# Optimization experiments

Measured on AMD Instinct MI355X. Metric: run time of the kernel, lower is better.

The kernel has to match this reference:

```python
import jax, jax.numpy as jnp
import numpy as np

EMB = 64
L = 2
NU = 100000
NI = 50000
ER = 1000000
ET = 800000
EP = 200000


def setup_inputs() -> dict:
    key = jax.random.key(0)
    ks = jax.random.split(key, 32)
    f = jnp.float32
    def nrm(k, shape, s=0.01):
        return (jax.random.normal(k, shape) * s).astype(f)
    inp = {}
    # graph structure (int)
    inp['rate_src'] = jax.random.randint(ks[0], (ER,), 0, NU)
    inp['rate_dst'] = jax.random.randint(ks[1], (ER,), 0, NI)
    inp['trust_src'] = jax.random.randint(ks[2], (ET,), 0, NU)
    inp['trust_dst'] = jax.random.randint(ks[3], (ET,), 0, NU)
    inp['pos_u'] = jax.random.randint(ks[4], (EP,), 0, NU)
    inp['pos_i'] = jax.random.randint(ks[5], (EP,), 0, NI)
    inp['neg_u'] = jax.random.randint(ks[6], (EP,), 0, NU)
    inp['neg_i'] = jax.random.randint(ks[7], (EP,), 0, NI)
    # embeddings (init normal(0, 0.01) per init_weights)
    inp['eu'] = nrm(ks[8], (NU, EMB))
    inp['ei'] = nrm(ks[9], (NI, EMB))
    # per-rel GATv2 params, stacked over L layers; [:,0]=fc_src, [:,1]=fc_dst
    inp['rate_W'] = nrm(ks[10], (L, 2, EMB, EMB))
    inp['rate_b'] = jnp.zeros((L, 2, EMB), f)
    inp['rate_attn'] = nrm(ks[11], (L, EMB), 0.1)
    inp['rate_bias'] = jnp.zeros((L, EMB), f)
    inp['rb_W'] = nrm(ks[12], (L, 2, EMB, EMB))
    inp['rb_b'] = jnp.zeros((L, 2, EMB), f)
    inp['rb_attn'] = nrm(ks[13], (L, EMB), 0.1)
    inp['rb_bias'] = jnp.zeros((L, EMB), f)
    inp['tr_W'] = nrm(ks[14], (L, 2, EMB, EMB))
    inp['tr_b'] = jnp.zeros((L, 2, EMB), f)
    inp['tr_attn'] = nrm(ks[15], (L, EMB), 0.1)
    inp['tr_bias'] = jnp.zeros((L, EMB), f)
    # attention-gate MLPs: [:, 0]=influence, [:, 1]=interest
    inp['attW1'] = nrm(ks[16], (L, 2, 2 * EMB, 2 * EMB))
    inp['attb1'] = jnp.zeros((L, 2, 2 * EMB), f)
    inp['attW2'] = nrm(ks[17], (L, 2, 2 * EMB))
    inp['attb2'] = jnp.zeros((L, 2), f)
    return inp


def gatv2(hs, hd, src, dst, Ws, bs, Wd, bd, attn, bias, n_dst):
    # DGL GATv2Conv, num_heads=1: e = attn . leaky_relu(Ws h_u + Wd h_v), slope 0.2
    fs = hs @ Ws + bs          # [Ns, E]
    fd = hd @ Wd + bd          # [Nd, E]
    e = jax.nn.leaky_relu(fs[src] + fd[dst], 0.2) @ attn  # [E]
    m = jax.ops.segment_max(e, dst, num_segments=n_dst)
    ex = jnp.exp(e - m[dst])
    denom = jax.ops.segment_sum(ex, dst, num_segments=n_dst)
    alpha = ex / denom[dst]
    out = jax.ops.segment_sum(alpha[:, None] * fs[src], dst, num_segments=n_dst)
    return out + bias


def _bn1(x):
    # BatchNorm1d(1), training-mode batch stats, affine identity at init
    mu = jnp.mean(x)
    var = jnp.mean((x - mu) ** 2)
    return (x - mu) * jax.lax.rsqrt(var + 1e-5)


def reference(eu, ei, rate_W, rate_b, rate_attn, rate_bias, rb_W, rb_b, rb_attn,
              rb_bias, tr_W, tr_b, tr_attn, tr_bias, attW1, attb1, attW2, attb2,
              rate_src, rate_dst, trust_src, trust_dst, pos_u, pos_i, neg_u, neg_i):
    n_users, n_items = eu.shape[0], ei.shape[0]
    hu, hi = eu, ei
    res_u, res_i = [eu], [ei]
    for l in range(rate_W.shape[0]):
        # interest diffusion: rate (user->item) and rated-by (item->user, reverse edges)
        hi_new = gatv2(hu, hi, rate_src, rate_dst, rate_W[l, 0], rate_b[l, 0],
                       rate_W[l, 1], rate_b[l, 1], rate_attn[l], rate_bias[l], n_items) + hi
        q = gatv2(hi, hu, rate_dst, rate_src, rb_W[l, 0], rb_b[l, 0],
                  rb_W[l, 1], rb_b[l, 1], rb_attn[l], rb_bias[l], n_users)
        # influence diffusion: trust (user->user)
        p = gatv2(hu, hu, trust_src, trust_dst, tr_W[l, 0], tr_b[l, 0],
                  tr_W[l, 1], tr_b[l, 1], tr_attn[l], tr_bias[l], n_users)
        def att(h2, i):
            z = (h2 @ attW1[l, i] + attb1[l, i]) @ attW2[l, i] + attb2[l, i]  # [N]
            return jax.nn.leaky_relu(_bn1(z), 0.01)
        a_inf = att(jnp.concatenate([hu, p], axis=1), 0)
        a_int = att(jnp.concatenate([hu, q], axis=1), 1)
        gamma = jax.nn.softmax(jnp.stack([a_inf, a_int], axis=1), axis=1)  # [N,2]
        hu = gamma[:, 0:1] * p + gamma[:, 1:2] * q + hu
        hi = hi_new
        res_u.append(hu)
        res_i.append(hi)
    hu_all = jnp.concatenate(res_u, axis=1)  # [NU, EMB*(1+L)]
    hi_all = jnp.concatenate(res_i, axis=1)
    pos = jnp.sum(hu_all[pos_u] * hi_all[pos_i], axis=1, keepdims=True)  # [EP,1]
    neg = jnp.sum(hu_all[neg_u] * hi_all[neg_i], axis=1, keepdims=True)
    return pos, neg
```

## Files before the change

kernel.cpp:

```cpp
#include <hip/hip_runtime.h>
#include <hip/hip_bf16.h>
#include <cstdint>

typedef __hip_bfloat16 bf16;
typedef __attribute__((ext_vector_type(8))) short frag_ab;
typedef __attribute__((ext_vector_type(4))) float frag_cd;
typedef __attribute__((ext_vector_type(4))) short short4v;

__device__ __forceinline__ float b2f(short s){
  return __uint_as_float(((unsigned)(unsigned short)s) << 16);
}

__device__ __forceinline__ void bf_split(float x, short& hi, short& lo){
  bf16 h = __float2bfloat16(x);
  float hf = __bfloat162float(h);
  bf16 l = __float2bfloat16(x - hf);
  __builtin_memcpy(&hi, &h, 2);
  __builtin_memcpy(&lo, &l, 2);
}

__device__ __forceinline__ float wave_sum(float v){
#pragma unroll
  for (int o = 32; o > 0; o >>= 1) v += __shfl_down(v, o, 64);
  return v;
}

__global__ void k_copy_in(const float* __restrict__ src, float* __restrict__ dst,
                          int n, int stride){
  int idx = blockIdx.x * 256 + threadIdx.x;
  if (idx >= n * 64) return;
  int r = idx >> 6, j = idx & 63;
  dst[(size_t)r * stride + j] = src[idx];
}

__global__ void k_linear(const float* __restrict__ x, int xs, int xo,
                         const float* __restrict__ W, const float* __restrict__ b,
                         bf16* __restrict__ out, int n){
  __shared__ float Wl[4096];
  int t = threadIdx.x;
  for (int i = t; i < 4096; i += 256) Wl[i] = W[i];
  __syncthreads();
  int lane = t & 63, w = t >> 6;
  int quad = lane >> 4, n16 = lane & 15;

  frag_ab bhi[4][2], blo[4][2];
#pragma unroll
  for (int c = 0; c < 4; ++c)
#pragma unroll
    for (int h = 0; h < 2; ++h){
      frag_ab vh, vl;
#pragma unroll
      for (int j = 0; j < 8; ++j){
        float wv = Wl[(32 * h + quad * 8 + j) * 64 + 16 * c + n16];
        short sh, sl; bf_split(wv, sh, sl);
        vh[j] = sh; vl[j] = sl;
      }
      bhi[c][h] = vh; blo[c][h] = vl;
    }
  float bj[4];
#pragma unroll
  for (int c = 0; c < 4; ++c) bj[c] = b[16 * c + n16];

  int rowbase = blockIdx.x * 64 + w * 16;
  if (rowbase >= n) return;
  int lrow = rowbase + n16; if (lrow >= n) lrow = n - 1;
  const float* xp = x + (size_t)lrow * xs + xo;
  frag_ab ahi[2], alo[2];
#pragma unroll
  for (int h = 0; h < 2; ++h){
    frag_ab vh, vl;
#pragma unroll
    for (int j = 0; j < 8; ++j){
      float xv = xp[32 * h + quad * 8 + j];
      short sh, sl; bf_split(xv, sh, sl);
      vh[j] = sh; vl[j] = sl;
    }
    ahi[h] = vh; alo[h] = vl;
  }
  frag_cd acc[4];
#pragma unroll
  for (int c = 0; c < 4; ++c) acc[c] = frag_cd{0.f, 0.f, 0.f, 0.f};
#pragma unroll
  for (int c = 0; c < 4; ++c)
#pragma unroll
    for (int h = 0; h < 2; ++h){
      acc[c] = __builtin_amdgcn_mfma_f32_16x16x32_bf16(ahi[h], bhi[c][h], acc[c], 0, 0, 0);
      acc[c] = __builtin_amdgcn_mfma_f32_16x16x32_bf16(alo[h], bhi[c][h], acc[c], 0, 0, 0);
      acc[c] = __builtin_amdgcn_mfma_f32_16x16x32_bf16(ahi[h], blo[c][h], acc[c], 0, 0, 0);
    }
#pragma unroll
  for (int reg = 0; reg < 4; ++reg){
    int r = rowbase + quad * 4 + reg;
    if (r >= n) continue;
#pragma unroll
    for (int c = 0; c < 4; ++c)
      out[(size_t)r * 64 + 16 * c + n16] = __float2bfloat16(acc[c][reg] + bj[c]);
  }
}

__global__ void k_hist(const int* __restrict__ dst, int* __restrict__ cnt, int E){
  int k = blockIdx.x * 256 + threadIdx.x;
  if (k < E) atomicAdd(cnt + dst[k], 1);
}
__global__ void k_hist2(const int* __restrict__ src, const int* __restrict__ dst,
                        int* __restrict__ cntA, int* __restrict__ cntB, int E){
  int k = blockIdx.x * 256 + threadIdx.x;
  if (k >= E) return;
  atomicAdd(cntA + dst[k], 1);
  atomicAdd(cntB + src[k], 1);
}

__global__ void k_scan_mb(const int* __restrict__ cnt, int n,
                          int* __restrict__ offs, int* __restrict__ cur,
                          int* __restrict__ gbase){
  __shared__ int wsum[16];
  __shared__ int base_sh;
  int t = threadIdx.x, lane = t & 63, w = t >> 6;
  int i = blockIdx.x * 1024 + t;
  int v = (i < n) ? cnt[i] : 0;
  int x = v;
#pragma unroll
  for (int o = 1; o < 64; o <<= 1){
    int y = __shfl_up(x, o, 64);
    if (lane >= o) x += y;
  }
  if (lane == 63) wsum[w] = x;
  __syncthreads();
  if (t == 0){
    int tot = 0;
    for (int k = 0; k < 16; ++k){ int c = wsum[k]; wsum[k] = tot; tot += c; }
    base_sh = atomicAdd(gbase, tot);
  }
  __syncthreads();
  if (i < n){
    int e = base_sh + wsum[w] + x - v;
    offs[i] = e; cur[i] = e;
  }
}

__global__ void k_csr_fill(const int* __restrict__ src, const int* __restrict__ dst,
                           int* __restrict__ cur, int* __restrict__ csr_src, int E){
  int t = blockIdx.x * 256 + threadIdx.x;
  int T = gridDim.x * 256;
  int k0 = t, k1 = t + T, k2 = t + 2 * T, k3 = t + 3 * T;
  bool b0 = k0 < E, b1 = k1 < E, b2 = k2 < E, b3 = k3 < E;
  int s0 = 0, d0 = 0, s1 = 0, d1 = 0, s2 = 0, d2 = 0, s3 = 0, d3 = 0;
  if (b0){ s0 = src[k0]; d0 = dst[k0]; }
  if (b1){ s1 = src[k1]; d1 = dst[k1]; }
  if (b2){ s2 = src[k2]; d2 = dst[k2]; }
  if (b3){ s3 = src[k3]; d3 = dst[k3]; }
  int p0 = 0, p1 = 0, p2 = 0, p3 = 0;
  if (b0) p0 = atomicAdd(cur + d0, 1);
  if (b1) p1 = atomicAdd(cur + d1, 1);
  if (b2) p2 = atomicAdd(cur + d2, 1);
  if (b3) p3 = atomicAdd(cur + d3, 1);
  if (b0) csr_src[p0] = s0;
  if (b1) csr_src[p1] = s1;
  if (b2) csr_src[p2] = s2;
  if (b3) csr_src[p3] = s3;
}
__global__ void k_csr_fill2(const int* __restrict__ src, const int* __restrict__ dst,
                            int* __restrict__ curA, int* __restrict__ csrA,
                            int* __restrict__ curB, int* __restrict__ csrB, int E){
  int t = blockIdx.x * 256 + threadIdx.x;
  int T = gridDim.x * 256;
  int k0 = t, k1 = t + T, k2 = t + 2 * T, k3 = t + 3 * T;
  bool b0 = k0 < E, b1 = k1 < E, b2 = k2 < E, b3 = k3 < E;
  int s0 = 0, d0 = 0, s1 = 0, d1 = 0, s2 = 0, d2 = 0, s3 = 0, d3 = 0;
  if (b0){ s0 = src[k0]; d0 = dst[k0]; }
  if (b1){ s1 = src[k1]; d1 = dst[k1]; }
  if (b2){ s2 = src[k2]; d2 = dst[k2]; }
  if (b3){ s3 = src[k3]; d3 = dst[k3]; }
  int pa0 = 0, pa1 = 0, pa2 = 0, pa3 = 0, pb0 = 0, pb1 = 0, pb2 = 0, pb3 = 0;
  if (b0) pa0 = atomicAdd(curA + d0, 1);
  if (b1) pa1 = atomicAdd(curA + d1, 1);
  if (b2) pa2 = atomicAdd(curA + d2, 1);
  if (b3) pa3 = atomicAdd(curA + d3, 1);
  if (b0) pb0 = atomicAdd(curB + s0, 1);
  if (b1) pb1 = atomicAdd(curB + s1, 1);
  if (b2) pb2 = atomicAdd(curB + s2, 1);
  if (b3) pb3 = atomicAdd(curB + s3, 1);
  if (b0){ csrA[pa0] = s0; csrB[pb0] = d0; }
  if (b1){ csrA[pa1] = s1; csrB[pb1] = d1; }
  if (b2){ csrA[pa2] = s2; csrB[pb2] = d2; }
  if (b3){ csrA[pa3] = s3; csrB[pb3] = d3; }
}

__global__ void k_gat(const int* __restrict__ offs, const int* __restrict__ cnt,
                      const int* __restrict__ csr_src,
                      const bf16* __restrict__ fs, const bf16* __restrict__ fd,
                      const float* __restrict__ attn, const float* __restrict__ bias,
                      float* __restrict__ out, int os, int oo,
                      const float* __restrict__ res, int rs, int ro, int n){
  int d = blockIdx.x * 4 + (threadIdx.x >> 6);
  if (d >= n) return;
  int lane = threadIdx.x & 63;
  int g = lane >> 4, l16 = lane & 15;
  short4v dv = *(const short4v*)(fd + (size_t)d * 64 + 4 * l16);
  float fd0 = b2f(dv[0]), fd1 = b2f(dv[1]), fd2 = b2f(dv[2]), fd3 = b2f(dv[3]);
  float4 a4 = *(const float4*)(attn + 4 * l16);
  float acc0 = 0.f, acc1 = 0.f, acc2 = 0.f, acc3 = 0.f, den = 0.f;
  int idx0 = offs[d], end = idx0 + cnt[d];
  for (int idx = idx0; idx < end; idx += 4){
    int e = idx + g;
    bool valid = e < end;
    int s = csr_src[valid ? e : idx];
    short4v sv = *(const short4v*)(fs + (size_t)s * 64 + 4 * l16);
    float f0 = b2f(sv[0]), f1 = b2f(sv[1]), f2 = b2f(sv[2]), f3 = b2f(sv[3]);
    float v0 = f0 + fd0; v0 = (v0 > 0.f ? v0 : 0.2f * v0) * a4.x;
    float v1 = f1 + fd1; v1 = (v1 > 0.f ? v1 : 0.2f * v1) * a4.y;
    float v2 = f2 + fd2; v2 = (v2 > 0.f ? v2 : 0.2f * v2) * a4.z;
    float v3 = f3 + fd3; v3 = (v3 > 0.f ? v3 : 0.2f * v3) * a4.w;
    float tt = (v0 + v1) + (v2 + v3);
#pragma unroll
    for (int o = 1; o < 16; o <<= 1) tt += __shfl_xor(tt, o, 64);
    float ex = valid ? __expf(tt) : 0.f;
    acc0 += ex * f0; acc1 += ex * f1; acc2 += ex * f2; acc3 += ex * f3;
    den += ex;
  }
#pragma unroll
  for (int o = 16; o < 64; o <<= 1){
    acc0 += __shfl_xor(acc0, o, 64); acc1 += __shfl_xor(acc1, o, 64);
    acc2 += __shfl_xor(acc2, o, 64); acc3 += __shfl_xor(acc3, o, 64);
    den  += __shfl_xor(den, o, 64);
  }
  if (g == 0){
    float4 b4 = *(const float4*)(bias + 4 * l16);
    float inv = (den > 0.f) ? 1.f / den : 0.f;
    float o0 = acc0 * inv + b4.x, o1 = acc1 * inv + b4.y;
    float o2 = acc2 * inv + b4.z, o3 = acc3 * inv + b4.w;
    if (res){
      float4 r4 = *(const float4*)(res + (size_t)d * rs + ro + 4 * l16);
      o0 += r4.x; o1 += r4.y; o2 += r4.z; o3 += r4.w;
    }
    *(float4*)(out + (size_t)d * os + oo + 4 * l16) = make_float4(o0, o1, o2, o3);
  }
}

__global__ void k_attvec(const float* __restrict__ W1, const float* __restrict__ b1,
                         const float* __restrict__ W2, const float* __restrict__ b2,
                         float* __restrict__ vvec, float* __restrict__ cs){
  int t = threadIdx.x;
  int li = t >> 7, r = t & 127;
  float acc = 0.f;
  for (int c = 0; c < 128; ++c)
    acc += W1[(size_t)(li * 128 + r) * 128 + c] * W2[li * 128 + c];
  vvec[li * 128 + r] = acc;
  if (r == 0){
    float cacc = b2[li];
    for (int c = 0; c < 128; ++c)
      cacc += b1[li * 128 + c] * W2[li * 128 + c];
    cs[li] = cacc;
  }
}

__global__ void k_gate_z(const float* __restrict__ hu_all, int l,
                         const float* __restrict__ p, const float* __restrict__ q,
                         const float* __restrict__ vvec, const float* __restrict__ cs,
                         float* __restrict__ z1, float* __restrict__ z2,
                         float* __restrict__ bsums, int n){
  __shared__ float part[4][4];
  int w = threadIdx.x >> 6, j = threadIdx.x & 63;
  int nidx = blockIdx.x * 4 + w;
  float lz1 = 0.f, lz2 = 0.f;
  if (nidx < n){
    const float* v1 = vvec + l * 256;
    const float* v2 = vvec + l * 256 + 128;
    float h  = hu_all[(size_t)nidx * 192 + l * 64 + j];
    float pv = p[(size_t)nidx * 64 + j];
    float qv = q[(size_t)nidx * 64 + j];
    float t1 = wave_sum(h * v1[j] + pv * v1[64 + j]);
    float t2 = wave_sum(h * v2[j] + qv * v2[64 + j]);
    if (j == 0){
      lz1 = t1 + cs[l * 2 + 0];
      lz2 = t2 + cs[l * 2 + 1];
      z1[nidx] = lz1;
      z2[nidx] = lz2;
    }
  }
  if (j == 0){
    part[w][0] = lz1; part[w][1] = lz1 * lz1;
    part[w][2] = lz2; part[w][3] = lz2 * lz2;
  }
  __syncthreads();
  if (threadIdx.x < 4)
    bsums[(size_t)blockIdx.x * 4 + threadIdx.x] =
        part[0][threadIdx.x] + part[1][threadIdx.x] +
        part[2][threadIdx.x] + part[3][threadIdx.x];
}

__global__ void k_bn_part(const float* __restrict__ bsums, int nb,
                          double* __restrict__ gpart){
  __shared__ double sh[256];
  int c = threadIdx.x & 3, r0 = blockIdx.x * 64 + (threadIdx.x >> 2);
  double acc = 0.0;
  for (int i = r0; i < nb; i += gridDim.x * 64)
    acc += (double)bsums[(size_t)i * 4 + c];
  sh[threadIdx.x] = acc;
  __syncthreads();
  for (int s = 128; s >= 4; s >>= 1){
    if (threadIdx.x < s) sh[threadIdx.x] += sh[threadIdx.x + s];
    __syncthreads();
  }
  if (threadIdx.x < 4) gpart[(size_t)blockIdx.x * 4 + threadIdx.x] = sh[threadIdx.x];
}

__global__ void k_bn_final(const double* __restrict__ gpart, int nbk,
                           double* __restrict__ sums){
  __shared__ double sh[256];
  int c = threadIdx.x & 3, k0 = threadIdx.x >> 2;
  double acc = 0.0;
  for (int i = k0; i < nbk; i += 64) acc += gpart[(size_t)i * 4 + c];
  sh[threadIdx.x] = acc;
  __syncthreads();
  for (int s = 128; s >= 4; s >>= 1){
    if (threadIdx.x < s) sh[threadIdx.x] += sh[threadIdx.x + s];
    __syncthreads();
  }
  if (threadIdx.x < 4) sums[threadIdx.x] = sh[threadIdx.x];
}

__global__ void k_gate_combine(float* __restrict__ hu_all, int l,
                               const float* __restrict__ p, const float* __restrict__ q,
                               const float* __restrict__ z1, const float* __restrict__ z2,
                               const double* __restrict__ sums, int n){
  int idx = blockIdx.x * 256 + threadIdx.x;
  if (idx >= n * 64) return;
  int r = idx >> 6, j = idx & 63;
  double invn = 1.0 / (double)n;
  double mu1 = sums[0] * invn, mu2 = sums[2] * invn;
  float var1 = (float)(sums[1] * invn - mu1 * mu1);
  float var2 = (float)(sums[3] * invn - mu2 * mu2);
  float rs1 = rsqrtf(var1 + 1e-5f), rs2 = rsqrtf(var2 + 1e-5f);
  float a1 = (z1[r] - (float)mu1) * rs1;
  float a2 = (z2[r] - (float)mu2) * rs2;
  a1 = a1 > 0.f ? a1 : 0.01f * a1;
  a2 = a2 > 0.f ? a2 : 0.01f * a2;
  float mx = fmaxf(a1, a2);
  float e1 = __expf(a1 - mx), e2 = __expf(a2 - mx);
  float inv = 1.f / (e1 + e2);
  float out = (e1 * inv) * p[idx] + (e2 * inv) * q[idx]
            + hu_all[(size_t)r * 192 + l * 64 + j];
  hu_all[(size_t)r * 192 + (l + 1) * 64 + j] = out;
}

__global__ void k_score(const int* __restrict__ pu, const int* __restrict__ pi,
                        const int* __restrict__ nu, const int* __restrict__ ni,
                        const float* __restrict__ hu_all, const float* __restrict__ hi_all,
                        float* __restrict__ out, int EP){
  int gw = blockIdx.x * 4 + (threadIdx.x >> 6);
  int sub = (threadIdx.x >> 4) & 3, l16 = threadIdx.x & 15;
  int k = gw * 4 + sub;
  if (k >= 2 * EP) return;
  int u, i;
  if (k < EP){ u = pu[k]; i = pi[k]; } else { u = nu[k - EP]; i = ni[k - EP]; }
  const float4* hu = (const float4*)(hu_all + (size_t)u * 192);
  const float4* hi = (const float4*)(hi_all + (size_t)i * 192);
  float acc = 0.f;
#pragma unroll
  for (int t = 0; t < 3; ++t){
    float4 a = hu[l16 + 16 * t];
    float4 b = hi[l16 + 16 * t];
    acc += a.x * b.x + a.y * b.y + a.z * b.z + a.w * b.w;
  }
#pragma unroll
  for (int o = 8; o > 0; o >>= 1) acc += __shfl_xor(acc, o, 64);
  if (l16 == 0) out[k] = acc;
}

extern "C" void kernel_launch(void* const* d_in, const int* in_sizes, int n_in,
                              void* d_out, int out_size, void* d_ws, size_t ws_size,
                              hipStream_t stream) {
  const int*   rate_src  = (const int*)  d_in[0];
  const int*   rate_dst  = (const int*)  d_in[1];
  const int*   trust_src = (const int*)  d_in[2];
  const int*   trust_dst = (const int*)  d_in[3];
  const int*   pos_u     = (const int*)  d_in[4];
  const int*   pos_i     = (const int*)  d_in[5];
  const int*   neg_u     = (const int*)  d_in[6];
  const int*   neg_i     = (const int*)  d_in[7];
  const float* eu        = (const float*)d_in[8];
  const float* ei        = (const float*)d_in[9];
  const float* rate_W    = (const float*)d_in[10];
  const float* rate_b    = (const float*)d_in[11];
  const float* rate_attn = (const float*)d_in[12];
  const float* rate_bias = (const float*)d_in[13];
  const float* rb_W      = (const float*)d_in[14];
  const float* rb_b      = (const float*)d_in[15];
  const float* rb_attn   = (const float*)d_in[16];
  const float* rb_bias   = (const float*)d_in[17];
  const float* tr_W      = (const float*)d_in[18];
  const float* tr_b      = (const float*)d_in[19];
  const float* tr_attn   = (const float*)d_in[20];
  const float* tr_bias   = (const float*)d_in[21];
  const float* attW1     = (const float*)d_in[22];
  const float* attb1     = (const float*)d_in[23];
  const float* attW2     = (const float*)d_in[24];
  const float* attb2     = (const float*)d_in[25];

  const int ER = in_sizes[0];
  const int ET = in_sizes[2];
  const int EP = in_sizes[4];
  const int NU = in_sizes[8] / 64;
  const int NI = in_sizes[9] / 64;

  float* ws = (float*)d_ws;
  float*  hu_all = ws;
  float*  hi_all = hu_all + (size_t)NU * 192;
  float*  p      = hi_all + (size_t)NI * 192;
  float*  q      = p + (size_t)NU * 64;
  bf16*   fs     = (bf16*)(q + (size_t)NU * 64);
  bf16*   fd     = (bf16*)(q + (size_t)NU * 128);
  float*  z1     = q + (size_t)NU * 192;
  float*  z2     = z1 + NU;
  float*  bsums  = z2 + NU;
  float*  vvec   = bsums + (size_t)(((NU + 3) / 4) * 4);
  float*  cs     = vvec + 512;
  double* sums   = (double*)(((uintptr_t)(cs + 4) + 15) & ~(uintptr_t)15);
  double* gpart  = sums + 4;
  int*    iw     = (int*)(gpart + 512);
  int*    cntA   = iw;
  int*    cntB   = cntA + NI;
  int*    cntC   = cntB + NU;
  int*    gbase  = cntC + NU;
  int*    offsA  = gbase + 4;
  int*    curA   = offsA + NI;
  int*    offsB  = curA + NI;
  int*    curB   = offsB + NU;
  int*    offsC  = curB + NU;
  int*    curC   = offsC + NU;
  int*    csrA   = curC + NU;
  int*    csrB   = csrA + ER;
  int*    csrC   = csrB + ER;

  auto cdiv = [](int a, int b){ return (a + b - 1) / b; };
  const int nbz = cdiv(NU, 4);

  k_copy_in<<<cdiv(NU * 64, 256), 256, 0, stream>>>(eu, hu_all, NU, 192);
  k_copy_in<<<cdiv(NI * 64, 256), 256, 0, stream>>>(ei, hi_all, NI, 192);
  k_attvec<<<1, 512, 0, stream>>>(attW1, attb1, attW2, attb2, vvec, cs);

  hipMemsetAsync(cntA, 0, (size_t)(NI + 2 * NU + 4) * 4, stream);
  k_hist2<<<cdiv(ER, 256), 256, 0, stream>>>(rate_src, rate_dst, cntA, cntB, ER);
  k_hist<<<cdiv(ET, 256), 256, 0, stream>>>(trust_dst, cntC, ET);
  k_scan_mb<<<cdiv(NI, 1024), 1024, 0, stream>>>(cntA, NI, offsA, curA, gbase + 0);
  k_scan_mb<<<cdiv(NU, 1024), 1024, 0, stream>>>(cntB, NU, offsB, curB, gbase + 1);
  k_scan_mb<<<cdiv(NU, 1024), 1024, 0, stream>>>(cntC, NU, offsC, curC, gbase + 2);
  k_csr_fill2<<<cdiv(ER, 1024), 256, 0, stream>>>(rate_src, rate_dst,
      curA, csrA, curB, csrB, ER);
  k_csr_fill<<<cdiv(ET, 1024), 256, 0, stream>>>(trust_src, trust_dst, curC, csrC, ET);

  for (int l = 0; l < 2; ++l){
    k_linear<<<cdiv(NU, 64), 256, 0, stream>>>(hu_all, 192, l * 64,
        rate_W + (size_t)(l * 2 + 0) * 4096, rate_b + (l * 2 + 0) * 64, fs, NU);
    k_linear<<<cdiv(NI, 64), 256, 0, stream>>>(hi_all, 192, l * 64,
        rate_W + (size_t)(l * 2 + 1) * 4096, rate_b + (l * 2 + 1) * 64, fd, NI);
    k_gat<<<cdiv(NI, 4), 256, 0, stream>>>(offsA, cntA, csrA, fs, fd,
        rate_attn + l * 64, rate_bias + l * 64,
        hi_all, 192, (l + 1) * 64, hi_all, 192, l * 64, NI);

    k_linear<<<cdiv(NI, 64), 256, 0, stream>>>(hi_all, 192, l * 64,
        rb_W + (size_t)(l * 2 + 0) * 4096, rb_b + (l * 2 + 0) * 64, fs, NI);
    k_linear<<<cdiv(NU, 64), 256, 0, stream>>>(hu_all, 192, l * 64,
        rb_W + (size_t)(l * 2 + 1) * 4096, rb_b + (l * 2 + 1) * 64, fd, NU);
    k_gat<<<cdiv(NU, 4), 256, 0, stream>>>(offsB, cntB, csrB, fs, fd,
        rb_attn + l * 64, rb_bias + l * 64,
        q, 64, 0, (const float*)nullptr, 0, 0, NU);

    k_linear<<<cdiv(NU, 64), 256, 0, stream>>>(hu_all, 192, l * 64,
        tr_W + (size_t)(l * 2 + 0) * 4096, tr_b + (l * 2 + 0) * 64, fs, NU);
    k_linear<<<cdiv(NU, 64), 256, 0, stream>>>(hu_all, 192, l * 64,
        tr_W + (size_t)(l * 2 + 1) * 4096, tr_b + (l * 2 + 1) * 64, fd, NU);
    k_gat<<<cdiv(NU, 4), 256, 0, stream>>>(offsC, cntC, csrC, fs, fd,
        tr_attn + l * 64, tr_bias + l * 64,
        p, 64, 0, (const float*)nullptr, 0, 0, NU);

    k_gate_z<<<nbz, 256, 0, stream>>>(hu_all, l, p, q, vvec, cs, z1, z2, bsums, NU);
    k_bn_part<<<128, 256, 0, stream>>>(bsums, nbz, gpart);
    k_bn_final<<<1, 256, 0, stream>>>(gpart, 128, sums);
    k_gate_combine<<<cdiv(NU * 64, 256), 256, 0, stream>>>(hu_all, l, p, q, z1, z2, sums, NU);
  }

  k_score<<<cdiv(2 * EP, 16), 256, 0, stream>>>(pos_u, pos_i, neg_u, neg_i,
      hu_all, hi_all, (float*)d_out, EP);
}
```

Measured before the change: 1.070 ms.

## Batch linear projections per input, pre-split weights, and drop second CSR atomic pass

```diff
diff --git a/kernel.cpp b/kernel.cpp
--- a/kernel.cpp
+++ b/kernel.cpp
@@ -10,7 +10,6 @@
 __device__ __forceinline__ float b2f(short s){
   return __uint_as_float(((unsigned)(unsigned short)s) << 16);
 }
-
 __device__ __forceinline__ void bf_split(float x, short& hi, short& lo){
   bf16 h = __float2bfloat16(x);
   float hf = __bfloat162float(h);
@@ -33,34 +32,31 @@
   dst[(size_t)r * stride + j] = src[idx];
 }
 
-__global__ void k_linear(const float* __restrict__ x, int xs, int xo,
-                         const float* __restrict__ W, const float* __restrict__ b,
-                         bf16* __restrict__ out, int n){
-  __shared__ float Wl[4096];
-  int t = threadIdx.x;
-  for (int i = t; i < 4096; i += 256) Wl[i] = W[i];
-  __syncthreads();
-  int lane = t & 63, w = t >> 6;
+__global__ void k_wsplit(const float* __restrict__ rateW, const float* __restrict__ rbW,
+                         const float* __restrict__ trW,
+                         short* __restrict__ Whi, short* __restrict__ Wlo){
+  int tid = blockIdx.x * 256 + threadIdx.x;
+  if (tid >= 12 * 4096) return;
+  int m = tid >> 12, rem = tid & 4095;
+  int lane = rem >> 6, rem2 = rem & 63;
+  int pair = rem2 >> 3, j = rem2 & 7;
+  int c = pair >> 1, h = pair & 1;
+  int rel = m >> 2, li = m & 3;
+  const float* base = (rel == 0) ? rateW : (rel == 1) ? rbW : trW;
+  float v = base[(size_t)li * 4096 + (32 * h + (lane >> 4) * 8 + j) * 64 + 16 * c + (lane & 15)];
+  short sh, sl; bf_split(v, sh, sl);
+  Whi[tid] = sh; Wlo[tid] = sl;
+}
+
+__global__ void k_linear_multi(const float* __restrict__ x, int xs, int xo, int n,
+                               const short* __restrict__ Whi, const short* __restrict__ Wlo,
+                               int mcount,
+                               int m0, const float* __restrict__ b0, bf16* __restrict__ o0,
+                               int m1, const float* __restrict__ b1, bf16* __restrict__ o1,
+                               int m2, const float* __restrict__ b2, bf16* __restrict__ o2,
+                               int m3, const float* __restrict__ b3, bf16* __restrict__ o3){
+  int lane = threadIdx.x & 63, w = threadIdx.x >> 6;
   int quad = lane >> 4, n16 = lane & 15;
-
-  frag_ab bhi[4][2], blo[4][2];
-#pragma unroll
-  for (int c = 0; c < 4; ++c)
-#pragma unroll
-    for (int h = 0; h < 2; ++h){
-      frag_ab vh, vl;
-#pragma unroll
-      for (int j = 0; j < 8; ++j){
-        float wv = Wl[(32 * h + quad * 8 + j) * 64 + 16 * c + n16];
-        short sh, sl; bf_split(wv, sh, sl);
-        vh[j] = sh; vl[j] = sl;
-      }
-      bhi[c][h] = vh; blo[c][h] = vl;
-    }
-  float bj[4];
-#pragma unroll
-  for (int c = 0; c < 4; ++c) bj[c] = b[16 * c + n16];
-
   int rowbase = blockIdx.x * 64 + w * 16;
   if (rowbase >= n) return;
   int lrow = rowbase + n16; if (lrow >= n) lrow = n - 1;
@@ -77,42 +73,54 @@
     }
     ahi[h] = vh; alo[h] = vl;
   }
-  frag_cd acc[4];
-#pragma unroll
-  for (int c = 0; c < 4; ++c) acc[c] = frag_cd{0.f, 0.f, 0.f, 0.f};
-#pragma unroll
-  for (int c = 0; c < 4; ++c)
-#pragma unroll
-    for (int h = 0; h < 2; ++h){
-      acc[c] = __builtin_amdgcn_mfma_f32_16x16x32_bf16(ahi[h], bhi[c][h], acc[c], 0, 0, 0);
-      acc[c] = __builtin_amdgcn_mfma_f32_16x16x32_bf16(alo[h], bhi[c][h], acc[c], 0, 0, 0);
-      acc[c] = __builtin_amdgcn_mfma_f32_16x16x32_bf16(ahi[h], blo[c][h], acc[c], 0, 0, 0);
+  int ms[4] = {m0, m1, m2, m3};
+  const float* bs[4] = {b0, b1, b2, b3};
+  bf16* os[4] = {o0, o1, o2, o3};
+  for (int i = 0; i < mcount; ++i){
+    const frag_ab* Bh = (const frag_ab*)(Whi + (size_t)ms[i] * 4096 + lane * 64);
+    const frag_ab* Bl = (const frag_ab*)(Wlo + (size_t)ms[i] * 4096 + lane * 64);
+    frag_cd acc[4];
+#pragma unroll
+    for (int c = 0; c < 4; ++c) acc[c] = frag_cd{0.f, 0.f, 0.f, 0.f};
+#pragma unroll
+    for (int c = 0; c < 4; ++c)
+#pragma unroll
+      for (int h = 0; h < 2; ++h){
+        frag_ab bh = Bh[c * 2 + h], bl = Bl[c * 2 + h];
+        acc[c] = __builtin_amdgcn_mfma_f32_16x16x32_bf16(ahi[h], bh, acc[c], 0, 0, 0);
+        acc[c] = __builtin_amdgcn_mfma_f32_16x16x32_bf16(alo[h], bh, acc[c], 0, 0, 0);
+        acc[c] = __builtin_amdgcn_mfma_f32_16x16x32_bf16(ahi[h], bl, acc[c], 0, 0, 0);
+      }
+    const float* bb = bs[i];
+    bf16* oo = os[i];
+#pragma unroll
+    for (int reg = 0; reg < 4; ++reg){
+      int r = rowbase + quad * 4 + reg;
+      if (r >= n) continue;
+#pragma unroll
+      for (int c = 0; c < 4; ++c)
+        oo[(size_t)r * 64 + 16 * c + n16] = __float2bfloat16(acc[c][reg] + bb[16 * c + n16]);
     }
-#pragma unroll
-  for (int reg = 0; reg < 4; ++reg){
-    int r = rowbase + quad * 4 + reg;
-    if (r >= n) continue;
-#pragma unroll
-    for (int c = 0; c < 4; ++c)
-      out[(size_t)r * 64 + 16 * c + n16] = __float2bfloat16(acc[c][reg] + bj[c]);
-  }
-}
-
-__global__ void k_hist(const int* __restrict__ dst, int* __restrict__ cnt, int E){
-  int k = blockIdx.x * 256 + threadIdx.x;
-  if (k < E) atomicAdd(cnt + dst[k], 1);
-}
-__global__ void k_hist2(const int* __restrict__ src, const int* __restrict__ dst,
-                        int* __restrict__ cntA, int* __restrict__ cntB, int E){
+  }
+}
+
+__global__ void k_hist2pos(const int* __restrict__ src, const int* __restrict__ dst,
+                           int* __restrict__ cntA, int* __restrict__ cntB,
+                           int* __restrict__ posA, int* __restrict__ posB, int E){
   int k = blockIdx.x * 256 + threadIdx.x;
   if (k >= E) return;
-  atomicAdd(cntA + dst[k], 1);
-  atomicAdd(cntB + src[k], 1);
+  posA[k] = atomicAdd(cntA + dst[k], 1);
+  posB[k] = atomicAdd(cntB + src[k], 1);
+}
+__global__ void k_histpos(const int* __restrict__ dst, int* __restrict__ cnt,
+                          int* __restrict__ pos, int E){
+  int k = blockIdx.x * 256 + threadIdx.x;
+  if (k >= E) return;
+  pos[k] = atomicAdd(cnt + dst[k], 1);
 }
 
 __global__ void k_scan_mb(const int* __restrict__ cnt, int n,
-                          int* __restrict__ offs, int* __restrict__ cur,
-                          int* __restrict__ gbase){
+                          int* __restrict__ offs, int* __restrict__ gbase){
   __shared__ int wsum[16];
   __shared__ int base_sh;
   int t = threadIdx.x, lane = t & 63, w = t >> 6;
@@ -132,58 +140,42 @@
     base_sh = atomicAdd(gbase, tot);
   }
   __syncthreads();
-  if (i < n){
-    int e = base_sh + wsum[w] + x - v;
-    offs[i] = e; cur[i] = e;
-  }
-}
-
-__global__ void k_csr_fill(const int* __restrict__ src, const int* __restrict__ dst,
-                           int* __restrict__ cur, int* __restrict__ csr_src, int E){
+  if (i < n) offs[i] = base_sh + wsum[w] + x - v;
+}
+
+__global__ void k_fill2_na(const int* __restrict__ src, const int* __restrict__ dst,
+                           const int* __restrict__ offsA, const int* __restrict__ posA,
+                           int* __restrict__ csrA,
+                           const int* __restrict__ offsB, const int* __restrict__ posB,
+                           int* __restrict__ csrB, int E){
   int t = blockIdx.x * 256 + threadIdx.x;
   int T = gridDim.x * 256;
-  int k0 = t, k1 = t + T, k2 = t + 2 * T, k3 = t + 3 * T;
-  bool b0 = k0 < E, b1 = k1 < E, b2 = k2 < E, b3 = k3 < E;
-  int s0 = 0, d0 = 0, s1 = 0, d1 = 0, s2 = 0, d2 = 0, s3 = 0, d3 = 0;
-  if (b0){ s0 = src[k0]; d0 = dst[k0]; }
-  if (b1){ s1 = src[k1]; d1 = dst[k1]; }
-  if (b2){ s2 = src[k2]; d2 = dst[k2]; }
-  if (b3){ s3 = src[k3]; d3 = dst[k3]; }
-  int p0 = 0, p1 = 0, p2 = 0, p3 = 0;
-  if (b0) p0 = atomicAdd(cur + d0, 1);
-  if (b1) p1 = atomicAdd(cur + d1, 1);
-  if (b2) p2 = atomicAdd(cur + d2, 1);
-  if (b3) p3 = atomicAdd(cur + d3, 1);
-  if (b0) csr_src[p0] = s0;
-  if (b1) csr_src[p1] = s1;
-  if (b2) csr_src[p2] = s2;
-  if (b3) csr_src[p3] = s3;
-}
-__global__ void k_csr_fill2(const int* __restrict__ src, const int* __restrict__ dst,
-                            int* __restrict__ curA, int* __restrict__ csrA,
-                            int* __restrict__ curB, int* __restrict__ csrB, int E){
+  int k0 = t, k1 = t + T;
+  bool b0 = k0 < E, b1 = k1 < E;
+  int s0 = 0, d0 = 0, s1 = 0, d1 = 0, p0 = 0, q0 = 0, p1 = 0, q1 = 0;
+  if (b0){ s0 = src[k0]; d0 = dst[k0]; p0 = posA[k0]; q0 = posB[k0]; }
+  if (b1){ s1 = src[k1]; d1 = dst[k1]; p1 = posA[k1]; q1 = posB[k1]; }
+  int oa0 = 0, ob0 = 0, oa1 = 0, ob1 = 0;
+  if (b0){ oa0 = offsA[d0]; ob0 = offsB[s0]; }
+  if (b1){ oa1 = offsA[d1]; ob1 = offsB[s1]; }
+  if (b0){ csrA[oa0 + p0] = s0; csrB[ob0 + q0] = d0; }
+  if (b1){ csrA[oa1 + p1] = s1; csrB[ob1 + q1] = d1; }
+}
+__global__ void k_fill_na(const int* __restrict__ src, const int* __restrict__ dst,
+                          const int* __restrict__ offs, const int* __restrict__ pos,
+                          int* __restrict__ csr, int E){
   int t = blockIdx.x * 256 + threadIdx.x;
   int T = gridDim.x * 256;
-  int k0 = t, k1 = t + T, k2 = t + 2 * T, k3 = t + 3 * T;
-  bool b0 = k0 < E, b1 = k1 < E, b2 = k2 < E, b3 = k3 < E;
-  int s0 = 0, d0 = 0, s1 = 0, d1 = 0, s2 = 0, d2 = 0, s3 = 0, d3 = 0;
-  if (b0){ s0 = src[k0]; d0 = dst[k0]; }
-  if (b1){ s1 = src[k1]; d1 = dst[k1]; }
-  if (b2){ s2 = src[k2]; d2 = dst[k2]; }
-  if (b3){ s3 = src[k3]; d3 = dst[k3]; }
-  int pa0 = 0, pa1 = 0, pa2 = 0, pa3 = 0, pb0 = 0, pb1 = 0, pb2 = 0, pb3 = 0;
-  if (b0) pa0 = atomicAdd(curA + d0, 1);
-  if (b1) pa1 = atomicAdd(curA + d1, 1);
-  if (b2) pa2 = atomicAdd(curA + d2, 1);
-  if (b3) pa3 = atomicAdd(curA + d3, 1);
-  if (b0) pb0 = atomicAdd(curB + s0, 1);
-  if (b1) pb1 = atomicAdd(curB + s1, 1);
-  if (b2) pb2 = atomicAdd(curB + s2, 1);
-  if (b3) pb3 = atomicAdd(curB + s3, 1);
-  if (b0){ csrA[pa0] = s0; csrB[pb0] = d0; }
-  if (b1){ csrA[pa1] = s1; csrB[pb1] = d1; }
-  if (b2){ csrA[pa2] = s2; csrB[pb2] = d2; }
-  if (b3){ csrA[pa3] = s3; csrB[pb3] = d3; }
+  int k0 = t, k1 = t + T;
+  bool b0 = k0 < E, b1 = k1 < E;
+  int s0 = 0, d0 = 0, p0 = 0, s1 = 0, d1 = 0, p1 = 0;
+  if (b0){ s0 = src[k0]; d0 = dst[k0]; p0 = pos[k0]; }
+  if (b1){ s1 = src[k1]; d1 = dst[k1]; p1 = pos[k1]; }
+  int o0 = 0, o1 = 0;
+  if (b0) o0 = offs[d0];
+  if (b1) o1 = offs[d1];
+  if (b0) csr[o0 + p0] = s0;
+  if (b1) csr[o1 + p1] = s1;
 }
 
 __global__ void k_gat(const int* __restrict__ offs, const int* __restrict__ cnt,
@@ -409,27 +401,34 @@
   float*  hi_all = hu_all + (size_t)NU * 192;
   float*  p      = hi_all + (size_t)NI * 192;
   float*  q      = p + (size_t)NU * 64;
-  bf16*   fs     = (bf16*)(q + (size_t)NU * 64);
-  bf16*   fd     = (bf16*)(q + (size_t)NU * 128);
-  float*  z1     = q + (size_t)NU * 192;
+  bf16*   tb     = (bf16*)(q + (size_t)NU * 64);
+  bf16*   fsA    = tb;
+  bf16*   fdB    = tb + (size_t)NU * 64;
+  bf16*   fsC    = tb + (size_t)NU * 128;
+  bf16*   fdC    = tb + (size_t)NU * 192;
+  bf16*   fdA    = (bf16*)p;
+  bf16*   fsB    = (bf16*)p + (size_t)NI * 64;
+  int*    posA   = (int*)fsA;
+  int*    posB   = (int*)fdB;
+  int*    posC   = (int*)fsC;
+  float*  z1     = (float*)(tb + (size_t)NU * 256);
   float*  z2     = z1 + NU;
   float*  bsums  = z2 + NU;
   float*  vvec   = bsums + (size_t)(((NU + 3) / 4) * 4);
   float*  cs     = vvec + 512;
   double* sums   = (double*)(((uintptr_t)(cs + 4) + 15) & ~(uintptr_t)15);
   double* gpart  = sums + 4;
-  int*    iw     = (int*)(gpart + 512);
+  short*  Whi    = (short*)(gpart + 512);
+  short*  Wlo    = Whi + 12 * 4096;
+  int*    iw     = (int*)(Wlo + 12 * 4096);
   int*    cntA   = iw;
   int*    cntB   = cntA + NI;
   int*    cntC   = cntB + NU;
   int*    gbase  = cntC + NU;
   int*    offsA  = gbase + 4;
-  int*    curA   = offsA + NI;
-  int*    offsB  = curA + NI;
-  int*    curB   = offsB + NU;
-  int*    offsC  = curB + NU;
-  int*    curC   = offsC + NU;
-  int*    csrA   = curC + NU;
+  int*    offsB  = offsA + NI;
+  int*    offsC  = offsB + NU;
+  int*    csrA   = offsC + NU;
   int*    csrB   = csrA + ER;
   int*    csrC   = csrB + ER;
 
@@ -439,39 +438,39 @@
   k_copy_in<<<cdiv(NU * 64, 256), 256, 0, stream>>>(eu, hu_all, NU, 192);
   k_copy_in<<<cdiv(NI * 64, 256), 256, 0, stream>>>(ei, hi_all, NI, 192);
   k_attvec<<<1, 512, 0, stream>>>(attW1, attb1, attW2, attb2, vvec, cs);
+  k_wsplit<<<192, 256, 0, stream>>>(rate_W, rb_W, tr_W, Whi, Wlo);
 
   hipMemsetAsync(cntA, 0, (size_t)(NI + 2 * NU + 4) * 4, stream);
-  k_hist2<<<cdiv(ER, 256), 256, 0, stream>>>(rate_src, rate_dst, cntA, cntB, ER);
-  k_hist<<<cdiv(ET, 256), 256, 0, stream>>>(trust_dst, cntC, ET);
-  k_scan_mb<<<cdiv(NI, 1024), 1024, 0, stream>>>(cntA, NI, offsA, curA, gbase + 0);
-  k_scan_mb<<<cdiv(NU, 1024), 1024, 0, stream>>>(cntB, NU, offsB, curB, gbase + 1);
-  k_scan_mb<<<cdiv(NU, 1024), 1024, 0, stream>>>(cntC, NU, offsC, curC, gbase + 2);
-  k_csr_fill2<<<cdiv(ER, 1024), 256, 0, stream>>>(rate_src, rate_dst,
-      curA, csrA, curB, csrB, ER);
-  k_csr_fill<<<cdiv(ET, 1024), 256, 0, stream>>>(trust_src, trust_dst, curC, csrC, ET);
+  k_hist2pos<<<cdiv(ER, 256), 256, 0, stream>>>(rate_src, rate_dst, cntA, cntB,
+                                                posA, posB, ER);
+  k_histpos<<<cdiv(ET, 256), 256, 0, stream>>>(trust_dst, cntC, posC, ET);
+  k_scan_mb<<<cdiv(NI, 1024), 1024, 0, stream>>>(cntA, NI, offsA, gbase + 0);
+  k_scan_mb<<<cdiv(NU, 1024), 1024, 0, stream>>>(cntB, NU, offsB, gbase + 1);
+  k_scan_mb<<<cdiv(NU, 1024), 1024, 0, stream>>>(cntC, NU, offsC, gbase + 2);
+  k_fill2_na<<<cdiv(ER, 512), 256, 0, stream>>>(rate_src, rate_dst,
+      offsA, posA, csrA, offsB, posB, csrB, ER);
+  k_fill_na<<<cdiv(ET, 512), 256, 0, stream>>>(trust_src, trust_dst,
+      offsC, posC, csrC, ET);
 
   for (int l = 0; l < 2; ++l){
-    k_linear<<<cdiv(NU, 64), 256, 0, stream>>>(hu_all, 192, l * 64,
-        rate_W + (size_t)(l * 2 + 0) * 4096, rate_b + (l * 2 + 0) * 64, fs, NU);
-    k_linear<<<cdiv(NI, 64), 256, 0, stream>>>(hi_all, 192, l * 64,
-        rate_W + (size_t)(l * 2 + 1) * 4096, rate_b + (l * 2 + 1) * 64, fd, NI);
-    k_gat<<<cdiv(NI, 4), 256, 0, stream>>>(offsA, cntA, csrA, fs, fd,
+    k_linear_multi<<<cdiv(NU, 64), 256, 0, stream>>>(hu_all, 192, l * 64, NU, Whi, Wlo, 4,
+        0 + l * 2 + 0, rate_b + (l * 2 + 0) * 64, fsA,
+        4 + l * 2 + 1, rb_b   + (l * 2 + 1) * 64, fdB,
+        8 + l * 2 + 0, tr_b   + (l * 2 + 0) * 64, fsC,
+        8 + l * 2 + 1, tr_b   + (l * 2 + 1) * 64, fdC);
+    k_linear_multi<<<cdiv(NI, 64), 256, 0, stream>>>(hi_all, 192, l * 64, NI, Whi, Wlo, 2,
+        0 + l * 2 + 1, rate_b + (l * 2 + 1) * 64, fdA,
+        4 + l * 2 + 0, rb_b   + (l * 2 + 0) * 64, fsB,
+        0, (const float*)nullptr, (bf16*)nullptr,
+        0, (const float*)nullptr, (bf16*)nullptr);
+
+    k_gat<<<cdiv(NI, 4), 256, 0, stream>>>(offsA, cntA, csrA, fsA, fdA,
         rate_attn + l * 64, rate_bias + l * 64,
         hi_all, 192, (l + 1) * 64, hi_all, 192, l * 64, NI);
-
-    k_linear<<<cdiv(NI, 64), 256, 0, stream>>>(hi_all, 192, l * 64,
-        rb_W + (size_t)(l * 2 + 0) * 4096, rb_b + (l * 2 + 0) * 64, fs, NI);
-    k_linear<<<cdiv(NU, 64), 256, 0, stream>>>(hu_all, 192, l * 64,
-        rb_W + (size_t)(l * 2 + 1) * 4096, rb_b + (l * 2 + 1) * 64, fd, NU);
-    k_gat<<<cdiv(NU, 4), 256, 0, stream>>>(offsB, cntB, csrB, fs, fd,
+    k_gat<<<cdiv(NU, 4), 256, 0, stream>>>(offsB, cntB, csrB, fsB, fdB,
         rb_attn + l * 64, rb_bias + l * 64,
         q, 64, 0, (const float*)nullptr, 0, 0, NU);
-
-    k_linear<<<cdiv(NU, 64), 256, 0, stream>>>(hu_all, 192, l * 64,
-        tr_W + (size_t)(l * 2 + 0) * 4096, tr_b + (l * 2 + 0) * 64, fs, NU);
-    k_linear<<<cdiv(NU, 64), 256, 0, stream>>>(hu_all, 192, l * 64,
-        tr_W + (size_t)(l * 2 + 1) * 4096, tr_b + (l * 2 + 1) * 64, fd, NU);
-    k_gat<<<cdiv(NU, 4), 256, 0, stream>>>(offsC, cntC, csrC, fs, fd,
+    k_gat<<<cdiv(NU, 4), 256, 0, stream>>>(offsC, cntC, csrC, fsC, fdC,
         tr_attn + l * 64, tr_bias + l * 64,
         p, 64, 0, (const float*)nullptr, 0, 0, NU);
 
```

Result: faster. 1.009 ms (-5.7%).
